# Kernel optimization log

Hardware: AMD Instinct MI355X
Metric: run time of the kernel (lower is better)

Reference implementation:

```python
import jax, jax.numpy as jnp
import numpy as np

TEMPERATURE = 0.07
NEG = -9e15  # matches torch masked_fill value
EPS = 1e-8   # torch.nn.functional.cosine_similarity eps


def setup_inputs() -> dict:
    key = jax.random.key(0)
    k1, k2 = jax.random.split(key)
    B, D = 4096, 512
    return {
        "feats1": jax.random.normal(k1, (B, D), dtype=jnp.float32),
        "feats2": jax.random.normal(k2, (B, D), dtype=jnp.float32),
    }


def reference(feats1, feats2):
    feats = jnp.concatenate([feats1, feats2], axis=0)            # [2N, D]
    n = feats.shape[0]
    # cosine similarity via normalize-once + GEMM (same math as the
    # broadcasted F.cosine_similarity, incl. per-vector eps clamp)
    norms = jnp.maximum(jnp.linalg.norm(feats, axis=-1, keepdims=True), EPS)
    fn = feats / norms                                            # [2N, D]
    cos_sim = fn @ fn.T                                           # [2N, 2N]
    # mask self-similarity BEFORE temperature division (as in torch code)
    idx = jnp.arange(n)
    cos_sim = jnp.where(idx[:, None] == idx[None, :], NEG, cos_sim)
    cos_sim = cos_sim / TEMPERATURE
    # positive pair: eye rolled by N rows -> column (i + N) mod 2N
    pos_idx = (idx + n // 2) % n
    pos = cos_sim[idx, pos_idx]                                   # [2N]
    nll = jnp.mean(-pos + jax.nn.logsumexp(cos_sim, axis=-1))
    # ranking: rank of the positive among [pos, masked negatives];
    # equals # of masked entries strictly greater than pos
    masked = jnp.where(idx[None, :] == pos_idx[:, None], NEG, cos_sim)
    rank = jnp.sum(masked > pos[:, None], axis=-1)                # int [2N]
    acc_top1 = jnp.mean((rank == 0).astype(jnp.float32))
    acc_top5 = jnp.mean((rank < 5).astype(jnp.float32))
    acc_mean_pos = 1.0 + jnp.mean(rank.astype(jnp.float32))
    return (nll, acc_top1, acc_top5, acc_mean_pos)
```

## Files before the change

kernel.cpp:

```cpp
#include <hip/hip_runtime.h>
#include <math.h>
#include <stdint.h>

#define NTOT   8192
#define HALF_N 4096
#define DIM    512
#define INV_T  14.2857142857142857f
#define NTILE  64
#define NBLK   2080

using s16x8 = __attribute__((ext_vector_type(8))) short;
using f32x4 = __attribute__((ext_vector_type(4))) float;

__device__ unsigned short g_fnb[NTOT * DIM];
__device__ float g_pos[NTOT];
__device__ float g_ps[(size_t)NTILE * NTOT];
__device__ int   g_pc[(size_t)NTILE * NTOT];
__device__ float g_part4[32 * 4];
__device__ int   g_tick2;

__constant__ int c_pre[11] = {0,136,392,648,904,1040,1296,1552,1688,1944,2080};
__constant__ int c_gi[10]  = {0,0,0,0,1,1,1,2,2,3};
__constant__ int c_gj[10]  = {0,1,2,3,1,2,3,2,3,3};

__device__ __forceinline__ float bf2f(unsigned short u) {
  union { unsigned int i; float f; } v; v.i = ((unsigned int)u) << 16; return v.f;
}
__device__ __forceinline__ unsigned short f2bf(float x) {
  union { float f; unsigned int i; } v; v.f = x;
  unsigned int u = v.i;
  return (unsigned short)((u + 0x7FFFu + ((u >> 16) & 1u)) >> 16);
}

__device__ __forceinline__ void gload16(const unsigned short* g, unsigned short* l) {
  __builtin_amdgcn_global_load_lds(
      (const __attribute__((address_space(1))) unsigned int*)g,
      (__attribute__((address_space(3))) unsigned int*)l, 16, 0, 0);
}

__global__ __launch_bounds__(256) void knorm(const float* __restrict__ f1,
                                             const float* __restrict__ f2) {
  const int tid  = threadIdx.x;
  const int wv   = tid >> 6;
  const int pi   = wv >> 1;
  const int half = wv & 1;
  const int lane = tid & 63;
  const int b    = blockIdx.x * 2 + pi;
  const int row  = b + half * HALF_N;

  if (blockIdx.x == 0 && tid == 0)
    __hip_atomic_store(&g_tick2, 0, __ATOMIC_RELAXED, __HIP_MEMORY_SCOPE_AGENT);

  const float* src = (half == 0) ? (f1 + (size_t)b * DIM) : (f2 + (size_t)b * DIM);
  float4 v0 = ((const float4*)src)[lane];
  float4 v1 = ((const float4*)src)[lane + 64];
  float ss = v0.x*v0.x + v0.y*v0.y + v0.z*v0.z + v0.w*v0.w
           + v1.x*v1.x + v1.y*v1.y + v1.z*v1.z + v1.w*v1.w;
  #pragma unroll
  for (int o = 32; o >= 1; o >>= 1) ss += __shfl_xor(ss, o, 64);
  const float sc = 1.0f / fmaxf(sqrtf(ss), 1e-8f);
  ushort4 h0, h1;
  h0.x = f2bf(v0.x * sc); h0.y = f2bf(v0.y * sc);
  h0.z = f2bf(v0.z * sc); h0.w = f2bf(v0.w * sc);
  h1.x = f2bf(v1.x * sc); h1.y = f2bf(v1.y * sc);
  h1.z = f2bf(v1.z * sc); h1.w = f2bf(v1.w * sc);
  ushort4* dst = (ushort4*)(g_fnb + (size_t)row * DIM);
  dst[lane]      = h0;
  dst[lane + 64] = h1;

  __shared__ ushort4 sh[2][64][2];
  if (half == 1) { sh[pi][lane][0] = h0; sh[pi][lane][1] = h1; }
  __syncthreads();
  if (half == 0) {
    const ushort4 p0 = sh[pi][lane][0], p1 = sh[pi][lane][1];
    float s = bf2f(h0.x)*bf2f(p0.x) + bf2f(h0.y)*bf2f(p0.y)
            + bf2f(h0.z)*bf2f(p0.z) + bf2f(h0.w)*bf2f(p0.w)
            + bf2f(h1.x)*bf2f(p1.x) + bf2f(h1.y)*bf2f(p1.y)
            + bf2f(h1.z)*bf2f(p1.z) + bf2f(h1.w)*bf2f(p1.w);
    #pragma unroll
    for (int o = 32; o >= 1; o >>= 1) s += __shfl_xor(s, o, 64);
    if (lane == 0) { g_pos[b] = s; g_pos[b + HALF_N] = s; }
  }
}

__global__ __launch_bounds__(256, 4) void kmain() {
  __shared__ __align__(16) unsigned short As[128 * 64];
  __shared__ __align__(16) unsigned short Bs[128 * 64];
  float* sRowS = reinterpret_cast<float*>(As);
  int*   sRowC = reinterpret_cast<int*>(sRowS + 128);
  float* sColS = reinterpret_cast<float*>(sRowC + 128);
  int*   sColC = reinterpret_cast<int*>(sColS + 128);

  const int t_sw = (blockIdx.x & 7) * (NBLK / 8) + (blockIdx.x >> 3);
  int sp = 0;
  while (t_sw >= c_pre[sp + 1]) ++sp;
  int l = t_sw - c_pre[sp];
  int lbi, lbj;
  if (c_gi[sp] == c_gj[sp]) {
    int r16 = 16; lbi = 0;
    while (l >= r16) { l -= r16; --r16; ++lbi; }
    lbj = lbi + l;
  } else {
    lbi = l >> 4; lbj = l & 15;
  }
  const int bi = c_gi[sp] * 16 + lbi;
  const int bj = c_gj[sp] * 16 + lbj;
  const bool offdiag = (bi != bj);
  const int i0 = bi * 128, j0 = bj * 128;

  const int tid  = threadIdx.x;
  const int lane = tid & 63;
  const int w    = tid >> 6;
  const int wr   = (w >> 1) * 64;
  const int wc   = (w & 1) * 64;
  const int lrow = lane & 15;
  const int lq   = lane >> 4;

  const int rsub = lane >> 3;
  const int lcb  = (lane & 7) ^ rsub;
  const unsigned short* Ag = g_fnb + (size_t)(i0 + w * 32 + rsub) * DIM + lcb * 8;
  const unsigned short* Bg = g_fnb + (size_t)(j0 + w * 32 + rsub) * DIM + lcb * 8;
  unsigned short* Al = &As[w * 32 * 64];
  unsigned short* Bl = &Bs[w * 32 * 64];

  f32x4 acc[4][4];
  #pragma unroll
  for (int a = 0; a < 4; ++a)
    #pragma unroll
    for (int bb = 0; bb < 4; ++bb) { acc[a][bb][0]=0.f; acc[a][bb][1]=0.f; acc[a][bb][2]=0.f; acc[a][bb][3]=0.f; }

  const unsigned short* Bls = offdiag ? (const unsigned short*)Bs
                                      : (const unsigned short*)As;

  for (int kt = 0; kt < 8; ++kt) {
    __syncthreads();
    const int kb = kt * 64;
    #pragma unroll
    for (int q = 0; q < 4; ++q) {
      gload16(Ag + (size_t)(q * 8) * DIM + kb, Al + q * 512);
      if (offdiag) gload16(Bg + (size_t)(q * 8) * DIM + kb, Bl + q * 512);
    }
    __syncthreads();

    #pragma unroll
    for (int kk = 0; kk < 2; ++kk) {
      s16x8 af[4], bf[4];
      #pragma unroll
      for (int mi = 0; mi < 4; ++mi) {
        const int r = wr + mi * 16 + lrow;
        af[mi] = *(const s16x8*)(&As[r * 64 + (((kk * 4 + lq) ^ (lrow & 7)) * 8)]);
      }
      #pragma unroll
      for (int ni = 0; ni < 4; ++ni) {
        const int r = wc + ni * 16 + lrow;
        bf[ni] = *(const s16x8*)(&Bls[r * 64 + (((kk * 4 + lq) ^ (lrow & 7)) * 8)]);
      }
      #pragma unroll
      for (int mi = 0; mi < 4; ++mi)
        #pragma unroll
        for (int ni = 0; ni < 4; ++ni)
          acc[mi][ni] = __builtin_amdgcn_mfma_f32_16x16x32_bf16(af[mi], bf[ni], acc[mi][ni], 0, 0, 0);
    }
  }

  __syncthreads();
  if (tid < 128) { sRowS[tid] = 0.f; sRowC[tid] = 0; sColS[tid] = 0.f; sColC[tid] = 0; }
  __syncthreads();

  #pragma unroll
  for (int mi = 0; mi < 4; ++mi) {
    #pragma unroll
    for (int r = 0; r < 4; ++r) {
      const int ridx = wr + mi * 16 + lq * 4 + r;
      const int i  = i0 + ridx;
      const float pv = g_pos[i];
      float s = 0.f; int c = 0;
      #pragma unroll
      for (int ni = 0; ni < 4; ++ni) {
        const int j = j0 + wc + ni * 16 + lrow;
        const float v = acc[mi][ni][r];
        const float e = __expf(v * INV_T);
        const bool diag = (j == i);
        s += diag ? 0.f : e;
        c += (!diag && (j != (i ^ HALF_N)) && (v > pv)) ? 1 : 0;
      }
      #pragma unroll
      for (int o = 1; o < 16; o <<= 1) {
        s += __shfl_xor(s, o, 64);
        c += __shfl_xor(c, o, 64);
      }
      if (lrow == 0) {
        atomicAdd(&sRowS[ridx], s);
        atomicAdd(&sRowC[ridx], c);
      }
    }
  }

  if (offdiag) {
    #pragma unroll
    for (int ni = 0; ni < 4; ++ni) {
      const int cidx = wc + ni * 16 + lrow;
      const int j  = j0 + cidx;
      const float pj = g_pos[j];
      float s = 0.f; int c = 0;
      #pragma unroll
      for (int mi = 0; mi < 4; ++mi) {
        #pragma unroll
        for (int r = 0; r < 4; ++r) {
          const int i = i0 + wr + mi * 16 + lq * 4 + r;
          const float v = acc[mi][ni][r];
          s += __expf(v * INV_T);
          c += ((i != (j ^ HALF_N)) && (v > pj)) ? 1 : 0;
        }
      }
      s += __shfl_xor(s, 16, 64); s += __shfl_xor(s, 32, 64);
      c += __shfl_xor(c, 16, 64); c += __shfl_xor(c, 32, 64);
      if (lq == 0) {
        atomicAdd(&sColS[cidx], s);
        atomicAdd(&sColC[cidx], c);
      }
    }
  }
  __syncthreads();

  if (tid < 128) {
    g_ps[(size_t)bj * NTOT + i0 + tid] = sRowS[tid];
    g_pc[(size_t)bj * NTOT + i0 + tid] = sRowC[tid];
  } else if (offdiag && tid < 256) {
    const int r2 = tid - 128;
    g_ps[(size_t)bi * NTOT + j0 + r2] = sColS[r2];
    g_pc[(size_t)bi * NTOT + j0 + r2] = sColC[r2];
  }
}

__global__ __launch_bounds__(256) void kredfin(float* __restrict__ out) {
  const int tid = threadIdx.x;
  const int i = blockIdx.x * 256 + tid;
  float s = 0.f; int c = 0;
  #pragma unroll 8
  for (int sl = 0; sl < NTILE; ++sl) {
    s += g_ps[(size_t)sl * NTOT + i];
    c += g_pc[(size_t)sl * NTOT + i];
  }
  float nll = -g_pos[i] * INV_T + logf(s);
  float t1 = (c == 0) ? 1.f : 0.f;
  float t5 = (c < 5) ? 1.f : 0.f;
  float mr = (float)c;
  #pragma unroll
  for (int o = 32; o >= 1; o >>= 1) {
    nll += __shfl_xor(nll, o, 64);
    t1  += __shfl_xor(t1, o, 64);
    t5  += __shfl_xor(t5, o, 64);
    mr  += __shfl_xor(mr, o, 64);
  }
  __shared__ float red[4][4];
  const int wv = tid >> 6, lane = tid & 63;
  if (lane == 0) { red[wv][0] = nll; red[wv][1] = t1; red[wv][2] = t5; red[wv][3] = mr; }
  __syncthreads();
  if (tid == 0) {
    float a = 0.f, b = 0.f, cc = 0.f, d = 0.f;
    #pragma unroll
    for (int k = 0; k < 4; ++k) { a += red[k][0]; b += red[k][1]; cc += red[k][2]; d += red[k][3]; }
    g_part4[blockIdx.x * 4 + 0] = a;
    g_part4[blockIdx.x * 4 + 1] = b;
    g_part4[blockIdx.x * 4 + 2] = cc;
    g_part4[blockIdx.x * 4 + 3] = d;
    __builtin_amdgcn_fence(__ATOMIC_RELEASE, "agent");
    const int old = __hip_atomic_fetch_add(&g_tick2, 1,
                        __ATOMIC_RELAXED, __HIP_MEMORY_SCOPE_AGENT);
    if (old == 31) {
      __builtin_amdgcn_fence(__ATOMIC_ACQUIRE, "agent");
      float A = 0.f, B = 0.f, C = 0.f, D = 0.f;
      for (int k = 0; k < 32; ++k) {
        A += g_part4[k * 4 + 0];
        B += g_part4[k * 4 + 1];
        C += g_part4[k * 4 + 2];
        D += g_part4[k * 4 + 3];
      }
      out[0] = A / (float)NTOT;
      out[1] = B / (float)NTOT;
      out[2] = C / (float)NTOT;
      out[3] = 1.f + D / (float)NTOT;
    }
  }
}

extern "C" void kernel_launch(void* const* d_in, const int* in_sizes, int n_in,
                              void* d_out, int out_size, void* d_ws, size_t ws_size,
                              hipStream_t stream) {
  const float* f1 = (const float*)d_in[0];
  const float* f2 = (const float*)d_in[1];
  float* out = (float*)d_out;

  knorm  <<<dim3(2048), dim3(256), 0, stream>>>(f1, f2);
  kmain  <<<dim3(NBLK), dim3(256), 0, stream>>>();
  kredfin<<<dim3(32),   dim3(256), 0, stream>>>(out);
}
```

Baseline: 147.3 us.

## Fuse normalize, tile GEMM and reduction into one cooperative persistent kernel

Replaces the three launches (normalize, tiled similarity/stats, final reduction) with a single cooperative kernel. It uses grid-wide syncs between the phases and a grid-stride persistent loop over the symmetric tile schedule, with the grid sized from occupancy. The aim is to remove launch gaps and inter-kernel drain/fill. In exchange it adds grid-barrier cost and may lower the number of concurrent blocks on the GEMM phase (launch bounds 256,4). It falls back to the old three kernels if the cooperative launch fails.

```diff
diff --git a/kernel.cpp b/kernel.cpp
--- a/kernel.cpp
+++ b/kernel.cpp
@@ -1,6 +1,9 @@
 #include <hip/hip_runtime.h>
+#include <hip/hip_cooperative_groups.h>
 #include <math.h>
 #include <stdint.h>
+
+namespace cg = cooperative_groups;
 
 #define NTOT   8192
 #define HALF_N 4096
@@ -36,6 +39,260 @@
   __builtin_amdgcn_global_load_lds(
       (const __attribute__((address_space(1))) unsigned int*)g,
       (__attribute__((address_space(3))) unsigned int*)l, 16, 0, 0);
+}
+
+__global__ __launch_bounds__(256, 4) void kfused(const float* __restrict__ f1,
+                                                 const float* __restrict__ f2,
+                                                 float* __restrict__ out) {
+  __shared__ __align__(16) unsigned short As[128 * 64];
+  __shared__ __align__(16) unsigned short Bs[128 * 64];
+  float* sRowS = reinterpret_cast<float*>(As);
+  int*   sRowC = reinterpret_cast<int*>(sRowS + 128);
+  float* sColS = reinterpret_cast<float*>(sRowC + 128);
+  int*   sColC = reinterpret_cast<int*>(sColS + 128);
+  ushort4 (*sh)[64][2] = reinterpret_cast<ushort4 (*)[64][2]>(Bs);
+  float (*red)[4] = reinterpret_cast<float (*)[4]>(As);
+
+  const int tid  = threadIdx.x;
+  const int lane = tid & 63;
+  const int w    = tid >> 6;
+
+  if (blockIdx.x == 0 && tid == 0)
+    __hip_atomic_store(&g_tick2, 0, __ATOMIC_RELAXED, __HIP_MEMORY_SCOPE_AGENT);
+
+  {
+    const int pi   = w >> 1;
+    const int half = w & 1;
+    for (int b0 = blockIdx.x * 2; b0 < HALF_N; b0 += gridDim.x * 2) {
+      const int b   = b0 + pi;
+      const int row = b + half * HALF_N;
+      const float* src = (half == 0) ? (f1 + (size_t)b * DIM) : (f2 + (size_t)b * DIM);
+      float4 v0 = ((const float4*)src)[lane];
+      float4 v1 = ((const float4*)src)[lane + 64];
+      float ss = v0.x*v0.x + v0.y*v0.y + v0.z*v0.z + v0.w*v0.w
+               + v1.x*v1.x + v1.y*v1.y + v1.z*v1.z + v1.w*v1.w;
+      #pragma unroll
+      for (int o = 32; o >= 1; o >>= 1) ss += __shfl_xor(ss, o, 64);
+      const float sc = 1.0f / fmaxf(sqrtf(ss), 1e-8f);
+      ushort4 h0, h1;
+      h0.x = f2bf(v0.x * sc); h0.y = f2bf(v0.y * sc);
+      h0.z = f2bf(v0.z * sc); h0.w = f2bf(v0.w * sc);
+      h1.x = f2bf(v1.x * sc); h1.y = f2bf(v1.y * sc);
+      h1.z = f2bf(v1.z * sc); h1.w = f2bf(v1.w * sc);
+      ushort4* dst = (ushort4*)(g_fnb + (size_t)row * DIM);
+      dst[lane]      = h0;
+      dst[lane + 64] = h1;
+
+      if (half == 1) { sh[pi][lane][0] = h0; sh[pi][lane][1] = h1; }
+      __syncthreads();
+      if (half == 0) {
+        const ushort4 p0 = sh[pi][lane][0], p1 = sh[pi][lane][1];
+        float s = bf2f(h0.x)*bf2f(p0.x) + bf2f(h0.y)*bf2f(p0.y)
+                + bf2f(h0.z)*bf2f(p0.z) + bf2f(h0.w)*bf2f(p0.w)
+                + bf2f(h1.x)*bf2f(p1.x) + bf2f(h1.y)*bf2f(p1.y)
+                + bf2f(h1.z)*bf2f(p1.z) + bf2f(h1.w)*bf2f(p1.w);
+        #pragma unroll
+        for (int o = 32; o >= 1; o >>= 1) s += __shfl_xor(s, o, 64);
+        if (lane == 0) { g_pos[b] = s; g_pos[b + HALF_N] = s; }
+      }
+      __syncthreads();
+    }
+  }
+
+  cg::this_grid().sync();
+
+  const int wr   = (w >> 1) * 64;
+  const int wc   = (w & 1) * 64;
+  const int lrow = lane & 15;
+  const int lq   = lane >> 4;
+  const int rsub = lane >> 3;
+  const int lcb  = (lane & 7) ^ rsub;
+
+  for (int tt = blockIdx.x; tt < NBLK; tt += gridDim.x) {
+    const int t_sw = (tt & 7) * (NBLK / 8) + (tt >> 3);
+    int sp = 0;
+    while (t_sw >= c_pre[sp + 1]) ++sp;
+    int l = t_sw - c_pre[sp];
+    int lbi, lbj;
+    if (c_gi[sp] == c_gj[sp]) {
+      int r16 = 16; lbi = 0;
+      while (l >= r16) { l -= r16; --r16; ++lbi; }
+      lbj = lbi + l;
+    } else {
+      lbi = l >> 4; lbj = l & 15;
+    }
+    const int bi = c_gi[sp] * 16 + lbi;
+    const int bj = c_gj[sp] * 16 + lbj;
+    const bool offdiag = (bi != bj);
+    const int i0 = bi * 128, j0 = bj * 128;
+
+    const unsigned short* Ag = g_fnb + (size_t)(i0 + w * 32 + rsub) * DIM + lcb * 8;
+    const unsigned short* Bg = g_fnb + (size_t)(j0 + w * 32 + rsub) * DIM + lcb * 8;
+    unsigned short* Al = &As[w * 32 * 64];
+    unsigned short* Bl = &Bs[w * 32 * 64];
+
+    f32x4 acc[4][4];
+    #pragma unroll
+    for (int a = 0; a < 4; ++a)
+      #pragma unroll
+      for (int bb = 0; bb < 4; ++bb) { acc[a][bb][0]=0.f; acc[a][bb][1]=0.f; acc[a][bb][2]=0.f; acc[a][bb][3]=0.f; }
+
+    const unsigned short* Bls = offdiag ? (const unsigned short*)Bs
+                                        : (const unsigned short*)As;
+
+    for (int kt = 0; kt < 8; ++kt) {
+      __syncthreads();
+      const int kb = kt * 64;
+      #pragma unroll
+      for (int q = 0; q < 4; ++q) {
+        gload16(Ag + (size_t)(q * 8) * DIM + kb, Al + q * 512);
+        if (offdiag) gload16(Bg + (size_t)(q * 8) * DIM + kb, Bl + q * 512);
+      }
+      __syncthreads();
+
+      #pragma unroll
+      for (int kk = 0; kk < 2; ++kk) {
+        s16x8 af[4], bf[4];
+        #pragma unroll
+        for (int mi = 0; mi < 4; ++mi) {
+          const int r = wr + mi * 16 + lrow;
+          af[mi] = *(const s16x8*)(&As[r * 64 + (((kk * 4 + lq) ^ (lrow & 7)) * 8)]);
+        }
+        #pragma unroll
+        for (int ni = 0; ni < 4; ++ni) {
+          const int r = wc + ni * 16 + lrow;
+          bf[ni] = *(const s16x8*)(&Bls[r * 64 + (((kk * 4 + lq) ^ (lrow & 7)) * 8)]);
+        }
+        #pragma unroll
+        for (int mi = 0; mi < 4; ++mi)
+          #pragma unroll
+          for (int ni = 0; ni < 4; ++ni)
+            acc[mi][ni] = __builtin_amdgcn_mfma_f32_16x16x32_bf16(af[mi], bf[ni], acc[mi][ni], 0, 0, 0);
+      }
+    }
+
+    __syncthreads();
+    if (tid < 128) { sRowS[tid] = 0.f; sRowC[tid] = 0; sColS[tid] = 0.f; sColC[tid] = 0; }
+    __syncthreads();
+
+    #pragma unroll
+    for (int mi = 0; mi < 4; ++mi) {
+      #pragma unroll
+      for (int r = 0; r < 4; ++r) {
+        const int ridx = wr + mi * 16 + lq * 4 + r;
+        const int i  = i0 + ridx;
+        const float pv = g_pos[i];
+        float s = 0.f; int c = 0;
+        #pragma unroll
+        for (int ni = 0; ni < 4; ++ni) {
+          const int j = j0 + wc + ni * 16 + lrow;
+          const float v = acc[mi][ni][r];
+          const float e = __expf(v * INV_T);
+          const bool diag = (j == i);
+          s += diag ? 0.f : e;
+          c += (!diag && (j != (i ^ HALF_N)) && (v > pv)) ? 1 : 0;
+        }
+        #pragma unroll
+        for (int o = 1; o < 16; o <<= 1) {
+          s += __shfl_xor(s, o, 64);
+          c += __shfl_xor(c, o, 64);
+        }
+        if (lrow == 0) {
+          atomicAdd(&sRowS[ridx], s);
+          atomicAdd(&sRowC[ridx], c);
+        }
+      }
+    }
+
+    if (offdiag) {
+      #pragma unroll
+      for (int ni = 0; ni < 4; ++ni) {
+        const int cidx = wc + ni * 16 + lrow;
+        const int j  = j0 + cidx;
+        const float pj = g_pos[j];
+        float s = 0.f; int c = 0;
+        #pragma unroll
+        for (int mi = 0; mi < 4; ++mi) {
+          #pragma unroll
+          for (int r = 0; r < 4; ++r) {
+            const int i = i0 + wr + mi * 16 + lq * 4 + r;
+            const float v = acc[mi][ni][r];
+            s += __expf(v * INV_T);
+            c += ((i != (j ^ HALF_N)) && (v > pj)) ? 1 : 0;
+          }
+        }
+        s += __shfl_xor(s, 16, 64); s += __shfl_xor(s, 32, 64);
+        c += __shfl_xor(c, 16, 64); c += __shfl_xor(c, 32, 64);
+        if (lq == 0) {
+          atomicAdd(&sColS[cidx], s);
+          atomicAdd(&sColC[cidx], c);
+        }
+      }
+    }
+    __syncthreads();
+
+    if (tid < 128) {
+      g_ps[(size_t)bj * NTOT + i0 + tid] = sRowS[tid];
+      g_pc[(size_t)bj * NTOT + i0 + tid] = sRowC[tid];
+    } else if (offdiag && tid < 256) {
+      const int r2 = tid - 128;
+      g_ps[(size_t)bi * NTOT + j0 + r2] = sColS[r2];
+      g_pc[(size_t)bi * NTOT + j0 + r2] = sColC[r2];
+    }
+    __syncthreads();
+  }
+
+  cg::this_grid().sync();
+
+  for (int cb = blockIdx.x; cb < 32; cb += gridDim.x) {
+    const int i = cb * 256 + tid;
+    float s = 0.f; int c = 0;
+    #pragma unroll 8
+    for (int sl = 0; sl < NTILE; ++sl) {
+      s += g_ps[(size_t)sl * NTOT + i];
+      c += g_pc[(size_t)sl * NTOT + i];
+    }
+    float nll = -g_pos[i] * INV_T + logf(s);
+    float t1 = (c == 0) ? 1.f : 0.f;
+    float t5 = (c < 5) ? 1.f : 0.f;
+    float mr = (float)c;
+    #pragma unroll
+    for (int o = 32; o >= 1; o >>= 1) {
+      nll += __shfl_xor(nll, o, 64);
+      t1  += __shfl_xor(t1, o, 64);
+      t5  += __shfl_xor(t5, o, 64);
+      mr  += __shfl_xor(mr, o, 64);
+    }
+    if (lane == 0) { red[w][0] = nll; red[w][1] = t1; red[w][2] = t5; red[w][3] = mr; }
+    __syncthreads();
+    if (tid == 0) {
+      float a = 0.f, b = 0.f, cc = 0.f, d = 0.f;
+      #pragma unroll
+      for (int k = 0; k < 4; ++k) { a += red[k][0]; b += red[k][1]; cc += red[k][2]; d += red[k][3]; }
+      g_part4[cb * 4 + 0] = a;
+      g_part4[cb * 4 + 1] = b;
+      g_part4[cb * 4 + 2] = cc;
+      g_part4[cb * 4 + 3] = d;
+      __builtin_amdgcn_fence(__ATOMIC_RELEASE, "agent");
+      const int old = __hip_atomic_fetch_add(&g_tick2, 1,
+                          __ATOMIC_RELAXED, __HIP_MEMORY_SCOPE_AGENT);
+      if (old == 31) {
+        __builtin_amdgcn_fence(__ATOMIC_ACQUIRE, "agent");
+        float A = 0.f, B = 0.f, C = 0.f, D = 0.f;
+        for (int k = 0; k < 32; ++k) {
+          A += g_part4[k * 4 + 0];
+          B += g_part4[k * 4 + 1];
+          C += g_part4[k * 4 + 2];
+          D += g_part4[k * 4 + 3];
+        }
+        out[0] = A / (float)NTOT;
+        out[1] = B / (float)NTOT;
+        out[2] = C / (float)NTOT;
+        out[3] = 1.f + D / (float)NTOT;
+      }
+    }
+    __syncthreads();
+  }
 }
 
 __global__ __launch_bounds__(256) void knorm(const float* __restrict__ f1,
@@ -292,7 +549,28 @@
   const float* f2 = (const float*)d_in[1];
   float* out = (float*)d_out;
 
-  knorm  <<<dim3(2048), dim3(256), 0, stream>>>(f1, f2);
-  kmain  <<<dim3(NBLK), dim3(256), 0, stream>>>();
-  kredfin<<<dim3(32),   dim3(256), 0, stream>>>(out);
-}
+  static int s_grid = 0;
+  if (s_grid == 0) {
+    int nb = 0;
+    hipError_t oe = hipOccupancyMaxActiveBlocksPerMultiprocessor(&nb, kfused, 256, 0);
+    int ncu = 256;
+    hipDeviceProp_t prop;
+    int dev = 0;
+    if (hipGetDevice(&dev) == hipSuccess && hipGetDeviceProperties(&prop, dev) == hipSuccess)
+      ncu = prop.multiProcessorCount;
+    if (oe != hipSuccess || nb < 1) { nb = 1; }
+    long g = (long)nb * (long)ncu;
+    if (g > NBLK) g = NBLK;
+    if (g < 64) g = 64;
+    s_grid = (int)g;
+  }
+
+  void* args[] = { (void*)&f1, (void*)&f2, (void*)&out };
+  hipError_t e = hipLaunchCooperativeKernel((const void*)kfused, dim3(s_grid),
+                                            dim3(256), args, 0, stream);
+  if (e != hipSuccess) {
+    knorm  <<<dim3(2048), dim3(256), 0, stream>>>(f1, f2);
+    kmain  <<<dim3(NBLK), dim3(256), 0, stream>>>();
+    kredfin<<<dim3(32),   dim3(256), 0, stream>>>(out);
+  }
+}
```

Result: slower. 374.4 us (+154.2%).

## Load MFMA operands directly from global memory instead of staging through LDS

Applied to the files above, without the earlier changes.

Drops the shared-memory tiles and the global_load_lds staging with its two barriers per k-step. Each wave now reads its bf16 A/B fragments straight from global memory into registers and feeds MFMA over 16 unrolled k-steps. This removes LDS traffic and synchronisation, but each wave re-fetches operands that other waves share, so it relies on L1/L2 and loses the explicit data reuse.

```diff
diff --git a/kernel.cpp b/kernel.cpp
--- a/kernel.cpp
+++ b/kernel.cpp
@@ -30,12 +30,6 @@
   union { float f; unsigned int i; } v; v.f = x;
   unsigned int u = v.i;
   return (unsigned short)((u + 0x7FFFu + ((u >> 16) & 1u)) >> 16);
-}
-
-__device__ __forceinline__ void gload16(const unsigned short* g, unsigned short* l) {
-  __builtin_amdgcn_global_load_lds(
-      (const __attribute__((address_space(1))) unsigned int*)g,
-      (__attribute__((address_space(3))) unsigned int*)l, 16, 0, 0);
 }
 
 __global__ __launch_bounds__(256) void knorm(const float* __restrict__ f1,
@@ -84,12 +78,8 @@
 }
 
 __global__ __launch_bounds__(256, 4) void kmain() {
-  __shared__ __align__(16) unsigned short As[128 * 64];
-  __shared__ __align__(16) unsigned short Bs[128 * 64];
-  float* sRowS = reinterpret_cast<float*>(As);
-  int*   sRowC = reinterpret_cast<int*>(sRowS + 128);
-  float* sColS = reinterpret_cast<float*>(sRowC + 128);
-  int*   sColC = reinterpret_cast<int*>(sColS + 128);
+  __shared__ float sRowS[128]; __shared__ int sRowC[128];
+  __shared__ float sColS[128]; __shared__ int sColC[128];
 
   const int t_sw = (blockIdx.x & 7) * (NBLK / 8) + (blockIdx.x >> 3);
   int sp = 0;
@@ -116,12 +106,8 @@
   const int lrow = lane & 15;
   const int lq   = lane >> 4;
 
-  const int rsub = lane >> 3;
-  const int lcb  = (lane & 7) ^ rsub;
-  const unsigned short* Ag = g_fnb + (size_t)(i0 + w * 32 + rsub) * DIM + lcb * 8;
-  const unsigned short* Bg = g_fnb + (size_t)(j0 + w * 32 + rsub) * DIM + lcb * 8;
-  unsigned short* Al = &As[w * 32 * 64];
-  unsigned short* Bl = &Bs[w * 32 * 64];
+  const unsigned short* Ap = g_fnb + (size_t)(i0 + wr + lrow) * DIM + lq * 8;
+  const unsigned short* Bp = g_fnb + (size_t)(j0 + wc + lrow) * DIM + lq * 8;
 
   f32x4 acc[4][4];
   #pragma unroll
@@ -129,41 +115,23 @@
     #pragma unroll
     for (int bb = 0; bb < 4; ++bb) { acc[a][bb][0]=0.f; acc[a][bb][1]=0.f; acc[a][bb][2]=0.f; acc[a][bb][3]=0.f; }
 
-  const unsigned short* Bls = offdiag ? (const unsigned short*)Bs
-                                      : (const unsigned short*)As;
-
-  for (int kt = 0; kt < 8; ++kt) {
-    __syncthreads();
-    const int kb = kt * 64;
-    #pragma unroll
-    for (int q = 0; q < 4; ++q) {
-      gload16(Ag + (size_t)(q * 8) * DIM + kb, Al + q * 512);
-      if (offdiag) gload16(Bg + (size_t)(q * 8) * DIM + kb, Bl + q * 512);
-    }
-    __syncthreads();
-
-    #pragma unroll
-    for (int kk = 0; kk < 2; ++kk) {
-      s16x8 af[4], bf[4];
-      #pragma unroll
-      for (int mi = 0; mi < 4; ++mi) {
-        const int r = wr + mi * 16 + lrow;
-        af[mi] = *(const s16x8*)(&As[r * 64 + (((kk * 4 + lq) ^ (lrow & 7)) * 8)]);
-      }
-      #pragma unroll
-      for (int ni = 0; ni < 4; ++ni) {
-        const int r = wc + ni * 16 + lrow;
-        bf[ni] = *(const s16x8*)(&Bls[r * 64 + (((kk * 4 + lq) ^ (lrow & 7)) * 8)]);
-      }
-      #pragma unroll
-      for (int mi = 0; mi < 4; ++mi)
-        #pragma unroll
-        for (int ni = 0; ni < 4; ++ni)
-          acc[mi][ni] = __builtin_amdgcn_mfma_f32_16x16x32_bf16(af[mi], bf[ni], acc[mi][ni], 0, 0, 0);
-    }
-  }
-
-  __syncthreads();
+  #pragma unroll
+  for (int kt = 0; kt < 16; ++kt) {
+    const int ko = kt * 32;
+    s16x8 af[4], bf[4];
+    #pragma unroll
+    for (int mi = 0; mi < 4; ++mi)
+      af[mi] = *(const s16x8*)(Ap + (size_t)(mi * 16) * DIM + ko);
+    #pragma unroll
+    for (int ni = 0; ni < 4; ++ni)
+      bf[ni] = *(const s16x8*)(Bp + (size_t)(ni * 16) * DIM + ko);
+    #pragma unroll
+    for (int mi = 0; mi < 4; ++mi)
+      #pragma unroll
+      for (int ni = 0; ni < 4; ++ni)
+        acc[mi][ni] = __builtin_amdgcn_mfma_f32_16x16x32_bf16(af[mi], bf[ni], acc[mi][ni], 0, 0, 0);
+  }
+
   if (tid < 128) { sRowS[tid] = 0.f; sRowC[tid] = 0; sColS[tid] = 0.f; sColC[tid] = 0; }
   __syncthreads();
 
```

Result: slower. 232.8 us (+58.1%).

## Enlarge symmetric GEMM tiles to 256x256 with 512-thread blocks

Applied to the files above, without the earlier changes.

Grows each output tile of the symmetric similarity GEMM from 128x128 to 256x256, using 8 waves per block with each wave computing 128x64. The upper-triangle tile enumeration is simplified to a direct triangular walk over 32 tiles per side. This halves the number of partial row-sum slices that the reduction kernel must read, and it cuts global reloads of A and B. In exchange, register use per thread doubles for accumulators, occupancy drops, and there are only 528 blocks, which risks load imbalance across the CUs.

```diff
diff --git a/kernel.cpp b/kernel.cpp
--- a/kernel.cpp
+++ b/kernel.cpp
@@ -6,8 +6,8 @@
 #define HALF_N 4096
 #define DIM    512
 #define INV_T  14.2857142857142857f
-#define NTILE  64
-#define NBLK   2080
+#define NTILE  32
+#define NBLK   528
 
 using s16x8 = __attribute__((ext_vector_type(8))) short;
 using f32x4 = __attribute__((ext_vector_type(4))) float;
@@ -18,10 +18,6 @@
 __device__ int   g_pc[(size_t)NTILE * NTOT];
 __device__ float g_part4[32 * 4];
 __device__ int   g_tick2;
-
-__constant__ int c_pre[11] = {0,136,392,648,904,1040,1296,1552,1688,1944,2080};
-__constant__ int c_gi[10]  = {0,0,0,0,1,1,1,2,2,3};
-__constant__ int c_gj[10]  = {0,1,2,3,1,2,3,2,3,3};
 
 __device__ __forceinline__ float bf2f(unsigned short u) {
   union { unsigned int i; float f; } v; v.i = ((unsigned int)u) << 16; return v.f;
@@ -83,36 +79,26 @@
   }
 }
 
-__global__ __launch_bounds__(256, 4) void kmain() {
-  __shared__ __align__(16) unsigned short As[128 * 64];
-  __shared__ __align__(16) unsigned short Bs[128 * 64];
+__global__ __launch_bounds__(512, 2) void kmain() {
+  __shared__ __align__(16) unsigned short As[256 * 64];
+  __shared__ __align__(16) unsigned short Bs[256 * 64];
   float* sRowS = reinterpret_cast<float*>(As);
-  int*   sRowC = reinterpret_cast<int*>(sRowS + 128);
-  float* sColS = reinterpret_cast<float*>(sRowC + 128);
-  int*   sColC = reinterpret_cast<int*>(sColS + 128);
-
-  const int t_sw = (blockIdx.x & 7) * (NBLK / 8) + (blockIdx.x >> 3);
-  int sp = 0;
-  while (t_sw >= c_pre[sp + 1]) ++sp;
-  int l = t_sw - c_pre[sp];
-  int lbi, lbj;
-  if (c_gi[sp] == c_gj[sp]) {
-    int r16 = 16; lbi = 0;
-    while (l >= r16) { l -= r16; --r16; ++lbi; }
-    lbj = lbi + l;
-  } else {
-    lbi = l >> 4; lbj = l & 15;
-  }
-  const int bi = c_gi[sp] * 16 + lbi;
-  const int bj = c_gj[sp] * 16 + lbj;
+  int*   sRowC = reinterpret_cast<int*>(sRowS + 256);
+  float* sColS = reinterpret_cast<float*>(sRowC + 256);
+  int*   sColC = reinterpret_cast<int*>(sColS + 256);
+
+  int t = (blockIdx.x & 7) * (NBLK / 8) + (blockIdx.x >> 3);
+  int bi = 0, rem = NTILE;
+  while (t >= rem) { t -= rem; --rem; ++bi; }
+  const int bj = bi + t;
   const bool offdiag = (bi != bj);
-  const int i0 = bi * 128, j0 = bj * 128;
+  const int i0 = bi * 256, j0 = bj * 256;
 
   const int tid  = threadIdx.x;
   const int lane = tid & 63;
   const int w    = tid >> 6;
-  const int wr   = (w >> 1) * 64;
-  const int wc   = (w & 1) * 64;
+  const int wm   = w >> 2;
+  const int wn   = w & 3;
   const int lrow = lane & 15;
   const int lq   = lane >> 4;
 
@@ -123,9 +109,9 @@
   unsigned short* Al = &As[w * 32 * 64];
   unsigned short* Bl = &Bs[w * 32 * 64];
 
-  f32x4 acc[4][4];
-  #pragma unroll
-  for (int a = 0; a < 4; ++a)
+  f32x4 acc[8][4];
+  #pragma unroll
+  for (int a = 0; a < 8; ++a)
     #pragma unroll
     for (int bb = 0; bb < 4; ++bb) { acc[a][bb][0]=0.f; acc[a][bb][1]=0.f; acc[a][bb][2]=0.f; acc[a][bb][3]=0.f; }
 
@@ -144,19 +130,19 @@
 
     #pragma unroll
     for (int kk = 0; kk < 2; ++kk) {
-      s16x8 af[4], bf[4];
-      #pragma unroll
-      for (int mi = 0; mi < 4; ++mi) {
-        const int r = wr + mi * 16 + lrow;
+      s16x8 af[8], bf[4];
+      #pragma unroll
+      for (int mi = 0; mi < 8; ++mi) {
+        const int r = wm * 128 + mi * 16 + lrow;
         af[mi] = *(const s16x8*)(&As[r * 64 + (((kk * 4 + lq) ^ (lrow & 7)) * 8)]);
       }
       #pragma unroll
       for (int ni = 0; ni < 4; ++ni) {
-        const int r = wc + ni * 16 + lrow;
+        const int r = wn * 64 + ni * 16 + lrow;
         bf[ni] = *(const s16x8*)(&Bls[r * 64 + (((kk * 4 + lq) ^ (lrow & 7)) * 8)]);
       }
       #pragma unroll
-      for (int mi = 0; mi < 4; ++mi)
+      for (int mi = 0; mi < 8; ++mi)
         #pragma unroll
         for (int ni = 0; ni < 4; ++ni)
           acc[mi][ni] = __builtin_amdgcn_mfma_f32_16x16x32_bf16(af[mi], bf[ni], acc[mi][ni], 0, 0, 0);
@@ -164,20 +150,21 @@
   }
 
   __syncthreads();
-  if (tid < 128) { sRowS[tid] = 0.f; sRowC[tid] = 0; sColS[tid] = 0.f; sColC[tid] = 0; }
-  __syncthreads();
-
-  #pragma unroll
-  for (int mi = 0; mi < 4; ++mi) {
+  if (tid < 256) { sRowS[tid] = 0.f; sRowC[tid] = 0; }
+  else           { sColS[tid - 256] = 0.f; sColC[tid - 256] = 0; }
+  __syncthreads();
+
+  #pragma unroll
+  for (int mi = 0; mi < 8; ++mi) {
     #pragma unroll
     for (int r = 0; r < 4; ++r) {
-      const int ridx = wr + mi * 16 + lq * 4 + r;
+      const int ridx = wm * 128 + mi * 16 + lq * 4 + r;
       const int i  = i0 + ridx;
       const float pv = g_pos[i];
       float s = 0.f; int c = 0;
       #pragma unroll
       for (int ni = 0; ni < 4; ++ni) {
-        const int j = j0 + wc + ni * 16 + lrow;
+        const int j = j0 + wn * 64 + ni * 16 + lrow;
         const float v = acc[mi][ni][r];
         const float e = __expf(v * INV_T);
         const bool diag = (j == i);
@@ -199,15 +186,15 @@
   if (offdiag) {
     #pragma unroll
     for (int ni = 0; ni < 4; ++ni) {
-      const int cidx = wc + ni * 16 + lrow;
+      const int cidx = wn * 64 + ni * 16 + lrow;
       const int j  = j0 + cidx;
       const float pj = g_pos[j];
       float s = 0.f; int c = 0;
       #pragma unroll
-      for (int mi = 0; mi < 4; ++mi) {
+      for (int mi = 0; mi < 8; ++mi) {
         #pragma unroll
         for (int r = 0; r < 4; ++r) {
-          const int i = i0 + wr + mi * 16 + lq * 4 + r;
+          const int i = i0 + wm * 128 + mi * 16 + lq * 4 + r;
           const float v = acc[mi][ni][r];
           s += __expf(v * INV_T);
           c += ((i != (j ^ HALF_N)) && (v > pj)) ? 1 : 0;
@@ -223,11 +210,11 @@
   }
   __syncthreads();
 
-  if (tid < 128) {
+  if (tid < 256) {
     g_ps[(size_t)bj * NTOT + i0 + tid] = sRowS[tid];
     g_pc[(size_t)bj * NTOT + i0 + tid] = sRowC[tid];
-  } else if (offdiag && tid < 256) {
-    const int r2 = tid - 128;
+  } else if (offdiag) {
+    const int r2 = tid - 256;
     g_ps[(size_t)bi * NTOT + j0 + r2] = sColS[r2];
     g_pc[(size_t)bi * NTOT + j0 + r2] = sColC[r2];
   }
@@ -293,6 +280,6 @@
   float* out = (float*)d_out;
 
   knorm  <<<dim3(2048), dim3(256), 0, stream>>>(f1, f2);
-  kmain  <<<dim3(NBLK), dim3(256), 0, stream>>>();
+  kmain  <<<dim3(NBLK), dim3(512), 0, stream>>>();
   kredfin<<<dim3(32),   dim3(256), 0, stream>>>(out);
 }
```

Result: slower. 180.0 us (+22.2%).
